# Kernel optimization log

Measured on AMD Instinct MI355X. Metric: run time of the kernel, lower is better.

The kernel has to match this reference:

```python
import jax, jax.numpy as jnp
import numpy as np
from jax import lax

NPOINT = 1024
RADIUS = 0.4
NSAMPLE = 32
BN_EPS = 1e-5


def _square_distance(src, dst):
    # src [B,S,3], dst [B,N,3] -> [B,S,N]
    d = -2.0 * jnp.einsum('bsc,bnc->bsn', src, dst)
    d = d + jnp.sum(src ** 2, -1)[:, :, None]
    d = d + jnp.sum(dst ** 2, -1)[:, None, :]
    return d


def _farthest_point_sample(xyz, npoint):
    # xyz [B,N,3] -> int32 indices [B,npoint]
    B, N, _ = xyz.shape
    # deterministic start at index 0 (torch uses randint; math is otherwise identical)
    init_far = jnp.zeros((B,), dtype=jnp.int32)
    init_dist = jnp.full((B, N), 1e10, dtype=xyz.dtype)

    def step(carry, _):
        distance, farthest = carry
        centroid = jnp.take_along_axis(xyz, farthest[:, None, None], axis=1)  # [B,1,3]
        dist = jnp.sum((xyz - centroid) ** 2, -1)  # [B,N]
        distance = jnp.minimum(distance, dist)
        new_far = jnp.argmax(distance, axis=-1).astype(jnp.int32)
        return (distance, new_far), farthest

    (_, _), cents = lax.scan(step, (init_dist, init_far), None, length=npoint)
    return cents.T  # [B, npoint]


def _query_ball_point(radius, nsample, xyz, new_xyz):
    # xyz [B,N,3], new_xyz [B,S,3] -> idx [B,S,nsample]
    B, N, _ = xyz.shape
    sqr = _square_distance(new_xyz, xyz)  # [B,S,N]
    ar = jnp.arange(N, dtype=jnp.int32)
    gi = jnp.where(sqr > radius * radius, N, ar[None, None, :])
    gi = jnp.sort(gi, axis=-1)[:, :, :nsample]
    first = gi[:, :, :1]
    return jnp.where(gi == N, first, gi)


def setup_inputs() -> dict:
    key = jax.random.key(0)
    ks = jax.random.split(key, 8)
    B, N = 16, 4096
    inp = {
        'xyz': jax.random.normal(ks[0], (B, 3, N), jnp.float32),
        'points': jax.random.normal(ks[1], (B, 6, N), jnp.float32),
    }
    dims = [(64, 9), (64, 64), (128, 64)]
    for i, (o, c) in enumerate(dims):
        inp[f'w{i}'] = jax.random.normal(ks[2 + i], (o, c), jnp.float32) * 0.05
        inp[f'b{i}'] = jnp.zeros((o,), jnp.float32)
        inp[f'g{i}'] = jnp.ones((o,), jnp.float32)
        inp[f'beta{i}'] = jnp.zeros((o,), jnp.float32)
    return inp


def reference(xyz, points, w0, b0, g0, beta0, w1, b1, g1, beta1, w2, b2, g2, beta2):
    # xyz [B,3,N], points [B,6,N]
    xyz_t = jnp.transpose(xyz, (0, 2, 1))      # [B,N,3]
    pts_t = jnp.transpose(points, (0, 2, 1))   # [B,N,6]
    B, N, _ = xyz_t.shape
    S, ns = NPOINT, NSAMPLE

    fps_idx = _farthest_point_sample(xyz_t, S)                 # [B,S]
    new_xyz = jnp.take_along_axis(xyz_t, fps_idx[:, :, None], axis=1)  # [B,S,3]
    idx = _query_ball_point(RADIUS, ns, xyz_t, new_xyz)        # [B,S,ns]
    flat = idx.reshape(B, S * ns, 1)
    g_xyz = jnp.take_along_axis(xyz_t, flat, axis=1).reshape(B, S, ns, 3)
    g_xyz = g_xyz - new_xyz[:, :, None, :]                     # grouped_xyz_norm
    g_pts = jnp.take_along_axis(pts_t, flat, axis=1).reshape(B, S, ns, -1)
    feat = jnp.concatenate([g_xyz, g_pts], axis=-1)            # [B,S,ns,9]

    # shared MLP: 1x1 conv + BatchNorm (training-mode batch stats) + ReLU
    for w, b, g, be in ((w0, b0, g0, beta0), (w1, b1, g1, beta1), (w2, b2, g2, beta2)):
        h = jnp.einsum('bsnc,oc->bsno', feat, w) + b
        mu = jnp.mean(h, axis=(0, 1, 2))
        var = jnp.var(h, axis=(0, 1, 2))
        feat = jax.nn.relu((h - mu) * lax.rsqrt(var + BN_EPS) * g + be)

    new_points = jnp.max(feat, axis=2)                         # max over nsample -> [B,S,Cout]
    return (jnp.transpose(new_xyz, (0, 2, 1)), jnp.transpose(new_points, (0, 2, 1)))
```

## Files before the change

### kernel.cpp

```cpp
#include <hip/hip_runtime.h>
#include <hip/hip_bf16.h>
#include <stdint.h>

#define NB 16
#define NP 4096
#define NSP 1024
#define KNN 32
#define PTOT (NB*NSP*KNN)
#define NTILES (PTOT/16)

typedef __attribute__((ext_vector_type(8))) short short8;
typedef __attribute__((ext_vector_type(4))) float f32x4;

__device__ __forceinline__ float fadd_(float a,float b){return __fadd_rn(a,b);}
__device__ __forceinline__ float fmul_(float a,float b){return __fmul_rn(a,b);}
__device__ __forceinline__ float fsub_(float a,float b){return __fsub_rn(a,b);}

__device__ __forceinline__ float bf2f(unsigned short u){
    unsigned int x = ((unsigned int)u) << 16; float f; __builtin_memcpy(&f,&x,4); return f;
}
__device__ __forceinline__ unsigned short f2bf(float f){
    unsigned int x; __builtin_memcpy(&x,&f,4);
    x = x + 0x7fffu + ((x>>16)&1u);
    return (unsigned short)(x>>16);
}

template<int CTRL>
__device__ __forceinline__ unsigned long long dpp_max_step(unsigned long long v){
    unsigned int lo = (unsigned int)v, hi = (unsigned int)(v>>32);
    unsigned int lod = (unsigned int)__builtin_amdgcn_update_dpp(0, (int)lo, CTRL, 0xF, 0xF, true);
    unsigned int hid = (unsigned int)__builtin_amdgcn_update_dpp(0, (int)hi, CTRL, 0xF, 0xF, true);
    unsigned long long o = ((unsigned long long)hid<<32) | lod;
    return (o > v) ? o : v;
}

__global__ __launch_bounds__(512,1) void fps_kernel(const float* __restrict__ xyz,
    int* __restrict__ fps_idx)
{
    const int b = blockIdx.x, tid = threadIdx.x;
    const int lane = tid & 63, wv = tid >> 6;
    const float* xb = xyz + (size_t)b*3*NP;
    __shared__ float4 sp[NP];
    __shared__ unsigned long long slots[2][8];
    __shared__ int farr[NSP];
    float px[8],py[8],pz[8],pd[8];
    const int base = tid*8;
#pragma unroll
    for (int j=0;j<8;j+=4){
        float4 vx = *(const float4*)(xb + base + j);
        float4 vy = *(const float4*)(xb + NP + base + j);
        float4 vz = *(const float4*)(xb + 2*NP + base + j);
        px[j]=vx.x; px[j+1]=vx.y; px[j+2]=vx.z; px[j+3]=vx.w;
        py[j]=vy.x; py[j+1]=vy.y; py[j+2]=vy.z; py[j+3]=vy.w;
        pz[j]=vz.x; pz[j+1]=vz.y; pz[j+2]=vz.z; pz[j+3]=vz.w;
        sp[base+j+0] = make_float4(vx.x,vy.x,vz.x,0.f);
        sp[base+j+1] = make_float4(vx.y,vy.y,vz.y,0.f);
        sp[base+j+2] = make_float4(vx.z,vy.z,vz.z,0.f);
        sp[base+j+3] = make_float4(vx.w,vy.w,vz.w,0.f);
        pd[j]=1e10f; pd[j+1]=1e10f; pd[j+2]=1e10f; pd[j+3]=1e10f;
    }
    __syncthreads();
    int far = 0;
    float cx, cy, cz;
    { float4 c0 = sp[0]; cx=c0.x; cy=c0.y; cz=c0.z; }
    for (int s=0;s<NSP;s++){
        if (tid==0) farr[s]=far;
        float bd=-1.0f; int bi=0;
#pragma unroll
        for (int j=0;j<8;j++){
            float dx=fsub_(px[j],cx), dy=fsub_(py[j],cy), dz=fsub_(pz[j],cz);
            float d = fadd_(fadd_(fmul_(dx,dx),fmul_(dy,dy)),fmul_(dz,dz));
            float nd = fminf(pd[j], d); pd[j]=nd;
            if (nd > bd){ bd=nd; bi=base+j; }
        }
        unsigned int hb; __builtin_memcpy(&hb,&bd,4);
        unsigned long long best = ((unsigned long long)hb<<32) | (unsigned int)(NP-1-bi);
        best = dpp_max_step<0x111>(best);
        best = dpp_max_step<0x112>(best);
        best = dpp_max_step<0x114>(best);
        best = dpp_max_step<0x118>(best);
        best = dpp_max_step<0x142>(best);
        best = dpp_max_step<0x143>(best);
        if (lane==63) slots[s&1][wv] = best;
        __syncthreads();
        unsigned long long m = slots[s&1][0];
#pragma unroll
        for (int w=1;w<8;w++){ unsigned long long v = slots[s&1][w]; if (v > m) m = v; }
        far = NP-1-(int)(m & 0xFFFFFFFFu);
        float4 c = sp[far]; cx=c.x; cy=c.y; cz=c.z;
    }
    __syncthreads();
    for (int i=tid;i<NSP;i+=512) fps_idx[b*NSP+i] = farr[i];
}

__global__ void centroid_kernel(const float* __restrict__ xyz, const int* __restrict__ fps_idx,
    float* __restrict__ new_xyz, float* __restrict__ out0)
{
    int t = blockIdx.x*256 + threadIdx.x;
    if (t >= NB*NSP) return;
    int b = t>>10, s = t&1023;
    int id = fps_idx[t];
    const float* xb = xyz + (size_t)b*3*NP;
    float x=xb[id], y=xb[NP+id], z=xb[2*NP+id];
    float* nz = new_xyz + (size_t)t*3;
    nz[0]=x; nz[1]=y; nz[2]=z;
    out0[(size_t)b*3*NSP + s]         = x;
    out0[(size_t)b*3*NSP + NSP + s]   = y;
    out0[(size_t)b*3*NSP + 2*NSP + s] = z;
}

__global__ __launch_bounds__(256,1) void ball_gather_kernel(const float* __restrict__ xyz,
    const float* __restrict__ pts, const float* __restrict__ new_xyz,
    unsigned short* __restrict__ feat)
{
    const int lane = threadIdx.x & 63, wv = threadIdx.x >> 6;
    const int center = blockIdx.x*4 + wv;
    const int b = center >> 10;
    const float* xb = xyz + (size_t)b*3*NP;
    const float* pb = pts + (size_t)b*6*NP;
    const float* nz = new_xyz + (size_t)center*3;
    const float cx=nz[0], cy=nz[1], cz=nz[2];
    const float src2 = fadd_(fadd_(fmul_(cx,cx),fmul_(cy,cy)),fmul_(cz,cz));
    const float R2 = (float)(0.4*0.4);
    __shared__ int slots[4][32];
    int total = 0;
    for (int c0=0;c0<NP;c0+=64){
        const int i = c0 + lane;
        float x=xb[i], y=xb[NP+i], z=xb[2*NP+i];
        float dot  = fadd_(fadd_(fmul_(cx,x),fmul_(cy,y)),fmul_(cz,z));
        float dst2 = fadd_(fadd_(fmul_(x,x),fmul_(y,y)),fmul_(z,z));
        float d = fadd_(fadd_(fmul_(-2.0f,dot), src2), dst2);
        bool pred = !(d > R2);
        unsigned long long m = __ballot(pred);
        int pos = total + (int)__popcll(m & ((1ull<<lane)-1ull));
        if (pred && pos < 32) slots[wv][pos] = i;
        total += (int)__popcll(m);
        if (total >= 32) break;
    }
    const int nvalid = total < 32 ? total : 32;
    __syncthreads();
    const int n = lane & 31;
    const int idx = slots[wv][ (n < nvalid) ? n : 0 ];
    unsigned short* fr = feat + (size_t)center*KNN*32 + (size_t)n*32;
    if (lane < 32){
        float gx = fsub_(xb[idx], cx), gy = fsub_(xb[NP+idx], cy), gz = fsub_(xb[2*NP+idx], cz);
        float p0=pb[idx], p1=pb[NP+idx], p2=pb[2*NP+idx], p3=pb[3*NP+idx], p4=pb[4*NP+idx];
        short8 v;
        v[0]=(short)f2bf(gx); v[1]=(short)f2bf(gy); v[2]=(short)f2bf(gz);
        v[3]=(short)f2bf(p0); v[4]=(short)f2bf(p1); v[5]=(short)f2bf(p2);
        v[6]=(short)f2bf(p3); v[7]=(short)f2bf(p4);
        *(short8*)fr = v;
    } else {
        float p5 = pb[5*NP+idx];
        short8 v = (short8){0,0,0,0,0,0,0,0};
        v[0]=(short)f2bf(p5);
        *(short8*)(fr+8)  = v;
        short8 z8 = (short8){0,0,0,0,0,0,0,0};
        *(short8*)(fr+16) = z8;
        *(short8*)(fr+24) = z8;
    }
}

template<int KT,int OT,bool NORM_IN,bool STORE_H>
__global__ __launch_bounds__(256,1) void conv_kernel(const unsigned short* __restrict__ in,
    const unsigned short* __restrict__ wp, const float* __restrict__ bias,
    const float* __restrict__ nAB, unsigned short* __restrict__ h_out,
    double* __restrict__ stats)
{
    constexpr int K = KT*32, O = OT*16;
    const int lane = threadIdx.x & 63, wv = threadIdx.x >> 6;
    const int col = lane & 15, quad = lane >> 4;
    short8 bf[OT][KT];
#pragma unroll
    for (int t=0;t<OT;t++)
#pragma unroll
        for (int kt=0;kt<KT;kt++)
            bf[t][kt] = *(const short8*)(wp + (size_t)(t*16+col)*K + kt*32 + quad*8);
    float brow[OT];
#pragma unroll
    for (int t=0;t<OT;t++) brow[t] = bias[t*16+col];
    float nA[KT*8], nB[KT*8];
    if constexpr (NORM_IN){
#pragma unroll
        for (int kt=0;kt<KT;kt++)
#pragma unroll
            for (int j=0;j<8;j++){
                int c = kt*32+quad*8+j;
                nA[kt*8+j]=nAB[c]; nB[kt*8+j]=nAB[128+c];
            }
    }
    float ssum[OT], ssq[OT];
#pragma unroll
    for (int t=0;t<OT;t++){ ssum[t]=0.f; ssq[t]=0.f; }
    const int gw = blockIdx.x*4 + wv, nw = gridDim.x*4;
    for (int tile=gw; tile<NTILES; tile+=nw){
        const int row0 = tile*16;
        short8 af[KT];
#pragma unroll
        for (int kt=0;kt<KT;kt++){
            af[kt] = *(const short8*)(in + (size_t)(row0+col)*K + kt*32 + quad*8);
            if constexpr (NORM_IN){
#pragma unroll
                for (int j=0;j<8;j++){
                    float x = bf2f((unsigned short)af[kt][j]);
                    x = fmaxf(x*nA[kt*8+j]+nB[kt*8+j], 0.f);
                    af[kt][j] = (short)f2bf(x);
                }
            }
        }
        f32x4 acc[OT];
#pragma unroll
        for (int t=0;t<OT;t++) acc[t] = (f32x4){0.f,0.f,0.f,0.f};
#pragma unroll
        for (int kt=0;kt<KT;kt++)
#pragma unroll
            for (int t=0;t<OT;t++)
                acc[t] = __builtin_amdgcn_mfma_f32_16x16x32_bf16(af[kt], bf[t][kt], acc[t], 0,0,0);
#pragma unroll
        for (int t=0;t<OT;t++){
#pragma unroll
            for (int r=0;r<4;r++){
                float h = acc[t][r] + brow[t];
                if constexpr (STORE_H)
                    h_out[(size_t)(row0 + quad*4 + r)*O + t*16 + col] = f2bf(h);
                ssum[t] += h; ssq[t] = fmaf(h,h,ssq[t]);
            }
        }
    }
    __shared__ float bsum[128], bssq[128];
    for (int i=threadIdx.x;i<128;i+=256){ bsum[i]=0.f; bssq[i]=0.f; }
    __syncthreads();
#pragma unroll
    for (int t=0;t<OT;t++){
        float v = ssum[t]; v += __shfl_xor(v,16,64); v += __shfl_xor(v,32,64);
        float q = ssq[t];  q += __shfl_xor(q,16,64); q += __shfl_xor(q,32,64);
        if (quad==0){ atomicAdd(&bsum[t*16+col], v); atomicAdd(&bssq[t*16+col], q); }
    }
    __syncthreads();
    if ((int)threadIdx.x < O){
        const int slot = blockIdx.x & 7;
        atomicAdd(&stats[(size_t)(slot*2+0)*128 + threadIdx.x], (double)bsum[threadIdx.x]);
        atomicAdd(&stats[(size_t)(slot*2+1)*128 + threadIdx.x], (double)bssq[threadIdx.x]);
    }
}

__global__ void finalize_kernel(const double* __restrict__ stats, const float* __restrict__ g,
    const float* __restrict__ beta, float* __restrict__ AB, int O)
{
    int o = threadIdx.x;
    if (o >= O) return;
    double s=0.0, q=0.0;
#pragma unroll
    for (int slot=0;slot<8;slot++){
        s += stats[(size_t)(slot*2+0)*128+o];
        q += stats[(size_t)(slot*2+1)*128+o];
    }
    const double cnt = (double)PTOT;
    float mean = (float)(s/cnt);
    float var  = (float)(q/cnt - (s/cnt)*(s/cnt));
    float inv  = rsqrtf(var + 1e-5f);
    float A = g[o]*inv;
    AB[o] = A; AB[128+o] = beta[o] - mean*A;
}

__global__ __launch_bounds__(256,1) void conv_final_kernel(const unsigned short* __restrict__ in,
    const unsigned short* __restrict__ wp, const float* __restrict__ bias,
    const float* __restrict__ nABin, const float* __restrict__ nABout,
    float* __restrict__ out1)
{
    constexpr int KT=2, OT=8, K=64;
    const int lane = threadIdx.x & 63, wv = threadIdx.x >> 6;
    const int col = lane & 15, quad = lane >> 4;
    short8 bf[OT][KT];
#pragma unroll
    for (int t=0;t<OT;t++)
#pragma unroll
        for (int kt=0;kt<KT;kt++)
            bf[t][kt] = *(const short8*)(wp + (size_t)(t*16+col)*K + kt*32 + quad*8);
    float brow[OT], oA[OT], oB[OT];
#pragma unroll
    for (int t=0;t<OT;t++){
        brow[t] = bias[t*16+col];
        oA[t] = nABout[t*16+col];
        oB[t] = nABout[128+t*16+col];
    }
    float nA[16], nB[16];
#pragma unroll
    for (int kt=0;kt<2;kt++)
#pragma unroll
        for (int j=0;j<8;j++){
            int c = kt*32+quad*8+j;
            nA[kt*8+j]=nABin[c]; nB[kt*8+j]=nABin[128+c];
        }
    const int gw = blockIdx.x*4 + wv, nw = gridDim.x*4;
    for (int grp=gw; grp<NB*NSP; grp+=nw){
        float vmax[OT];
#pragma unroll
        for (int t=0;t<OT;t++) vmax[t]=0.f;
#pragma unroll
        for (int mt=0; mt<2; mt++){
            const int row0 = grp*32 + mt*16;
            short8 af[KT];
#pragma unroll
            for (int kt=0;kt<2;kt++){
                af[kt] = *(const short8*)(in + (size_t)(row0+col)*K + kt*32 + quad*8);
#pragma unroll
                for (int j=0;j<8;j++){
                    float x = bf2f((unsigned short)af[kt][j]);
                    x = fmaxf(x*nA[kt*8+j]+nB[kt*8+j], 0.f);
                    af[kt][j] = (short)f2bf(x);
                }
            }
            f32x4 acc[OT];
#pragma unroll
            for (int t=0;t<OT;t++) acc[t] = (f32x4){0.f,0.f,0.f,0.f};
#pragma unroll
            for (int kt=0;kt<2;kt++)
#pragma unroll
                for (int t=0;t<OT;t++)
                    acc[t] = __builtin_amdgcn_mfma_f32_16x16x32_bf16(af[kt], bf[t][kt], acc[t], 0,0,0);
#pragma unroll
            for (int t=0;t<OT;t++){
#pragma unroll
                for (int r=0;r<4;r++){
                    float h = acc[t][r] + brow[t];
                    float x = fmaxf(h*oA[t]+oB[t], 0.f);
                    vmax[t] = fmaxf(vmax[t], x);
                }
            }
        }
#pragma unroll
        for (int t=0;t<OT;t++){
            float v = vmax[t];
            v = fmaxf(v, __shfl_xor(v,16,64));
            v = fmaxf(v, __shfl_xor(v,32,64));
            if (quad==0){
                int o = t*16+col, bb = grp>>10, ss = grp&1023;
                out1[((size_t)bb*128+o)*NSP + ss] = v;
            }
        }
    }
}

__global__ void prep_kernel(const float* __restrict__ w0, const float* __restrict__ w1,
    const float* __restrict__ w2, unsigned short* __restrict__ wp0,
    unsigned short* __restrict__ wp1, unsigned short* __restrict__ wp2)
{
    int t = blockIdx.x*256 + threadIdx.x;
    if (t < 64*32){ int o=t>>5, c=t&31; wp0[t] = (c<9) ? f2bf(w0[o*9+c]) : (unsigned short)0; }
    if (t < 64*64)  wp1[t] = f2bf(w1[t]);
    if (t < 128*64) wp2[t] = f2bf(w2[t]);
}

extern "C" void kernel_launch(void* const* d_in, const int* in_sizes, int n_in,
                              void* d_out, int out_size, void* d_ws, size_t ws_size,
                              hipStream_t stream)
{
    (void)in_sizes; (void)n_in; (void)out_size; (void)ws_size;
    const float* xyz = (const float*)d_in[0];
    const float* pts = (const float*)d_in[1];
    const float* w0  = (const float*)d_in[2];
    const float* b0  = (const float*)d_in[3];
    const float* g0  = (const float*)d_in[4];
    const float* be0 = (const float*)d_in[5];
    const float* w1  = (const float*)d_in[6];
    const float* b1  = (const float*)d_in[7];
    const float* g1  = (const float*)d_in[8];
    const float* be1 = (const float*)d_in[9];
    const float* w2  = (const float*)d_in[10];
    const float* b2  = (const float*)d_in[11];
    const float* g2  = (const float*)d_in[12];
    const float* be2 = (const float*)d_in[13];

    char* ws = (char*)d_ws;
    size_t off = 0;
    auto alloc = [&](size_t sz)->char*{ char* p = ws + off; off = (off + sz + 255) & ~(size_t)255; return p; };
    int*            fps_idx = (int*)           alloc((size_t)NB*NSP*4);
    float*          new_xyz = (float*)         alloc((size_t)NB*NSP*3*4);
    unsigned short* wp0     = (unsigned short*)alloc(64*32*2);
    unsigned short* wp1     = (unsigned short*)alloc(64*64*2);
    unsigned short* wp2     = (unsigned short*)alloc(128*64*2);
    double*         stats   = (double*)        alloc((size_t)3*8*2*128*8);
    float*          AB0     = (float*)         alloc(256*4);
    float*          AB1     = (float*)         alloc(256*4);
    float*          AB2     = (float*)         alloc(256*4);
    unsigned short* feat    = (unsigned short*)alloc((size_t)PTOT*32*2);
    unsigned short* h0      = (unsigned short*)alloc((size_t)PTOT*64*2);
    unsigned short* h1      = (unsigned short*)alloc((size_t)PTOT*64*2);

    float* out0 = (float*)d_out;
    float* out1 = out0 + (size_t)NB*3*NSP;

    hipMemsetAsync(stats, 0, (size_t)3*8*2*128*8, stream);
    prep_kernel<<<32,256,0,stream>>>(w0,w1,w2,wp0,wp1,wp2);
    fps_kernel<<<NB,512,0,stream>>>(xyz, fps_idx);
    centroid_kernel<<<(NB*NSP+255)/256,256,0,stream>>>(xyz, fps_idx, new_xyz, out0);
    ball_gather_kernel<<<NB*NSP/4,256,0,stream>>>(xyz, pts, new_xyz, feat);
    conv_kernel<1,4,false,true><<<1024,256,0,stream>>>(feat, wp0, b0, nullptr, h0, stats);
    finalize_kernel<<<1,128,0,stream>>>(stats, g0, be0, AB0, 64);
    conv_kernel<2,4,true,true><<<1024,256,0,stream>>>(h0, wp1, b1, AB0, h1, stats + 2048);
    finalize_kernel<<<1,128,0,stream>>>(stats + 2048, g1, be1, AB1, 64);
    conv_kernel<2,8,true,false><<<1024,256,0,stream>>>(h1, wp2, b2, AB1, nullptr, stats + 4096);
    finalize_kernel<<<1,128,0,stream>>>(stats + 4096, g2, be2, AB2, 128);
    conv_final_kernel<<<2048,256,0,stream>>>(h1, wp2, b2, AB1, AB2, out1);
}
```

Before: 929.7 us.

## Halve FPS block size, process 16 points per thread with packed float2 math

The farthest-point-sampling kernel now runs with 256 threads (4 waves) per batch, and each thread holds 16 points instead of 8. Distance math uses two-wide float vectors so the compiler can emit packed FP32 instructions, with contraction disabled to keep exact rounding. The cross-wave reduction now reads 4 slots instead of 8, and indices are written straight to global memory instead of being staged in shared memory. The aim is to cut per-iteration barrier and reduction latency in this serial 1024-step loop, at the cost of more per-thread ALU work and register pressure.

Result: faster. 850.7 us (-8.5%).

```diff
diff --git a/kernel.cpp b/kernel.cpp
--- a/kernel.cpp
+++ b/kernel.cpp
@@ -11,6 +11,7 @@
 
 typedef __attribute__((ext_vector_type(8))) short short8;
 typedef __attribute__((ext_vector_type(4))) float f32x4;
+typedef __attribute__((ext_vector_type(2))) float f32x2;
 
 __device__ __forceinline__ float fadd_(float a,float b){return __fadd_rn(a,b);}
 __device__ __forceinline__ float fmul_(float a,float b){return __fmul_rn(a,b);}
@@ -34,25 +35,25 @@
     return (o > v) ? o : v;
 }
 
-__global__ __launch_bounds__(512,1) void fps_kernel(const float* __restrict__ xyz,
+__global__ __launch_bounds__(256,1) void fps_kernel(const float* __restrict__ xyz,
     int* __restrict__ fps_idx)
 {
     const int b = blockIdx.x, tid = threadIdx.x;
     const int lane = tid & 63, wv = tid >> 6;
     const float* xb = xyz + (size_t)b*3*NP;
     __shared__ float4 sp[NP];
-    __shared__ unsigned long long slots[2][8];
-    __shared__ int farr[NSP];
-    float px[8],py[8],pz[8],pd[8];
-    const int base = tid*8;
-#pragma unroll
-    for (int j=0;j<8;j+=4){
+    __shared__ unsigned long long slots[2][4];
+    f32x2 px[8], py[8], pz[8];
+    float pd[16];
+    const int base = tid*16;
+#pragma unroll
+    for (int j=0;j<16;j+=4){
         float4 vx = *(const float4*)(xb + base + j);
         float4 vy = *(const float4*)(xb + NP + base + j);
         float4 vz = *(const float4*)(xb + 2*NP + base + j);
-        px[j]=vx.x; px[j+1]=vx.y; px[j+2]=vx.z; px[j+3]=vx.w;
-        py[j]=vy.x; py[j+1]=vy.y; py[j+2]=vy.z; py[j+3]=vy.w;
-        pz[j]=vz.x; pz[j+1]=vz.y; pz[j+2]=vz.z; pz[j+3]=vz.w;
+        px[j/2]   = (f32x2){vx.x,vx.y}; px[j/2+1] = (f32x2){vx.z,vx.w};
+        py[j/2]   = (f32x2){vy.x,vy.y}; py[j/2+1] = (f32x2){vy.z,vy.w};
+        pz[j/2]   = (f32x2){vz.x,vz.y}; pz[j/2+1] = (f32x2){vz.z,vz.w};
         sp[base+j+0] = make_float4(vx.x,vy.x,vz.x,0.f);
         sp[base+j+1] = make_float4(vx.y,vy.y,vz.y,0.f);
         sp[base+j+2] = make_float4(vx.z,vy.z,vz.z,0.f);
@@ -64,14 +65,21 @@
     float cx, cy, cz;
     { float4 c0 = sp[0]; cx=c0.x; cy=c0.y; cz=c0.z; }
     for (int s=0;s<NSP;s++){
-        if (tid==0) farr[s]=far;
+        if (tid==0) fps_idx[b*NSP+s] = far;
         float bd=-1.0f; int bi=0;
-#pragma unroll
-        for (int j=0;j<8;j++){
-            float dx=fsub_(px[j],cx), dy=fsub_(py[j],cy), dz=fsub_(pz[j],cz);
-            float d = fadd_(fadd_(fmul_(dx,dx),fmul_(dy,dy)),fmul_(dz,dz));
-            float nd = fminf(pd[j], d); pd[j]=nd;
-            if (nd > bd){ bd=nd; bi=base+j; }
+        {
+#pragma clang fp contract(off)
+            const f32x2 cx2 = (f32x2){cx,cx}, cy2 = (f32x2){cy,cy}, cz2 = (f32x2){cz,cz};
+#pragma unroll
+            for (int k=0;k<8;k++){
+                f32x2 dx = px[k]-cx2, dy = py[k]-cy2, dz = pz[k]-cz2;
+                f32x2 d  = (dx*dx + dy*dy) + dz*dz;
+                float nd0 = fminf(pd[2*k],   d.x);
+                float nd1 = fminf(pd[2*k+1], d.y);
+                pd[2*k]=nd0; pd[2*k+1]=nd1;
+                if (nd0 > bd){ bd=nd0; bi=base+2*k;   }
+                if (nd1 > bd){ bd=nd1; bi=base+2*k+1; }
+            }
         }
         unsigned int hb; __builtin_memcpy(&hb,&bd,4);
         unsigned long long best = ((unsigned long long)hb<<32) | (unsigned int)(NP-1-bi);
@@ -83,14 +91,15 @@
         best = dpp_max_step<0x143>(best);
         if (lane==63) slots[s&1][wv] = best;
         __syncthreads();
-        unsigned long long m = slots[s&1][0];
-#pragma unroll
-        for (int w=1;w<8;w++){ unsigned long long v = slots[s&1][w]; if (v > m) m = v; }
-        far = NP-1-(int)(m & 0xFFFFFFFFu);
+        {
+            const unsigned long long* sl = slots[s&1];
+            unsigned long long a0 = sl[0], a1 = sl[1], a2 = sl[2], a3 = sl[3];
+            unsigned long long m0 = a0>a1?a0:a1, m1 = a2>a3?a2:a3;
+            unsigned long long m  = m0>m1?m0:m1;
+            far = NP-1-(int)(m & 0xFFFFFFFFu);
+        }
         float4 c = sp[far]; cx=c.x; cy=c.y; cz=c.z;
     }
-    __syncthreads();
-    for (int i=tid;i<NSP;i+=512) fps_idx[b*NSP+i] = farr[i];
 }
 
 __global__ void centroid_kernel(const float* __restrict__ xyz, const int* __restrict__ fps_idx,
@@ -393,7 +402,7 @@
 
     hipMemsetAsync(stats, 0, (size_t)3*8*2*128*8, stream);
     prep_kernel<<<32,256,0,stream>>>(w0,w1,w2,wp0,wp1,wp2);
-    fps_kernel<<<NB,512,0,stream>>>(xyz, fps_idx);
+    fps_kernel<<<NB,256,0,stream>>>(xyz, fps_idx);
     centroid_kernel<<<(NB*NSP+255)/256,256,0,stream>>>(xyz, fps_idx, new_xyz, out0);
     ball_gather_kernel<<<NB*NSP/4,256,0,stream>>>(xyz, pts, new_xyz, feat);
     conv_kernel<1,4,false,true><<<1024,256,0,stream>>>(feat, wp0, b0, nullptr, h0, stats);
```
